# Kernel optimization log

Measured on AMD Instinct MI355X. Metric: run time of the kernel, lower is better.

Reference implementation:

```python
import jax, jax.numpy as jnp
import numpy as np

NEG = -1e9  # soft -inf, fp16/bf16-safe-ish and avoids nan from inf-inf


def _nw_single(theta, A):
    """Soft Needleman-Wunsch (softmax operator = logsumexp merge).

    theta: [N, M] match scores, A: scalar gap score.
    V is conceptually an (N+1, M+1) grid with V[0,0]=0 and -inf boundaries:
      V[i, j] = theta[i-1, j-1] + lse(V[i-1, j] + A, V[i-1, j-1], V[i, j-1] + A)
    Computed wavefront-parallel over anti-diagonals d = i + j with lax.scan.
    Each diagonal is a length-(N+1) vector indexed by row i.
    Returns V[N, M].
    """
    N, M = theta.shape
    neg = jnp.asarray(NEG, theta.dtype)
    ii = jnp.arange(N)  # ii = i - 1 for active rows i = 1..N

    prev2 = jnp.full((N + 1,), neg, theta.dtype).at[0].set(0.0)  # diagonal d=0
    prev = jnp.full((N + 1,), neg, theta.dtype)                   # diagonal d=1

    def step(carry, d):
        p2, p1 = carry
        jj = d - ii - 2                       # column index j-1 on diagonal d
        valid = (jj >= 0) & (jj < M)
        th = theta[ii, jnp.clip(jj, 0, M - 1)]
        up = p1[:N] + A                        # V[i-1, j] + A
        diag = p2[:N]                          # V[i-1, j-1]
        left = p1[1:] + A                      # V[i, j-1] + A
        merged = jax.nn.logsumexp(jnp.stack([up, diag, left]), axis=0)
        newvals = jnp.where(valid, th + merged, neg)
        new = jnp.concatenate([neg[None], newvals])  # row i=0 is boundary
        return (p1, new), None

    ds = jnp.arange(2, N + M + 1)
    (_, last), _ = jax.lax.scan(step, (prev2, prev), ds)
    return last[N]  # V[N, M], terminal alignment score


def setup_inputs() -> dict:
    key = jax.random.key(0)
    k1, k2, k3 = jax.random.split(key, 3)
    B, N, M, D = 16, 1024, 1024, 512
    zx = jax.random.normal(k1, (B, N, D), dtype=jnp.float32)
    zy = jax.random.normal(k2, (B, M, D), dtype=jnp.float32)
    gap_w = jax.random.normal(k3, (1, 2 * D), dtype=jnp.float32) * (1.0 / np.sqrt(2 * D))
    gap_b = jnp.zeros((1,), dtype=jnp.float32)
    return {"zx": zx, "zy": zy, "gap_w": gap_w, "gap_b": gap_b}


def reference(zx, zy, gap_w, gap_b):
    # Pairwise match scores theta[b,i,j] = <zx[b,i], zy[b,j]>
    theta = jnp.einsum('bid,bjd->bij', zx, zy)
    # Per-pair scalar gap score from mean-pooled embeddings
    merged = jnp.concatenate([zx.mean(axis=1), zy.mean(axis=1)], axis=1)  # [B, 2D]
    A = (merged @ gap_w.T + gap_b)[:, 0]                                   # [B]
    # Soft NW alignment score per batch element
    return jax.vmap(_nw_single)(theta, A)                                  # [B]
```

## Files before the change

### kernel.cpp

```cpp
#include <hip/hip_runtime.h>
#include <hip/hip_bf16.h>

#define BATCH 16
#define NN 1024
#define MM 1024
#define DD 512

#define LOG2E 1.4426950408889634f
#define LN2f  0.6931471805599453f
#define NEGS  -1.442695e9f

#define DSTAG 128
#define GTOT  1480
#define PF    8

typedef __bf16 v8bf __attribute__((ext_vector_type(8)));
typedef __bf16 v4bf __attribute__((ext_vector_type(4)));
typedef float  v4f  __attribute__((ext_vector_type(4)));

__global__ void zero_acc(float* a) {
    if (threadIdx.x < BATCH) a[threadIdx.x] = 0.0f;
}

__global__ __launch_bounds__(256) void conv_reduce(
        const float* __restrict__ zx, const float* __restrict__ zy,
        const float* __restrict__ gw,
        __bf16* __restrict__ zxb, __bf16* __restrict__ zyb,
        float* __restrict__ acc) {
    const int chunk = blockIdx.x, b = blockIdx.y, which = blockIdx.z;
    const float* src = which ? zy : zx;
    __bf16* dst = which ? zyb : zxb;
    const float* g = gw + which * DD;
    const size_t base = ((size_t)b * NN + (size_t)chunk * 64) * DD;
    const int t = threadIdx.x;
    const int col = (t * 4) & (DD - 1);
    const float4 gv = *(const float4*)(g + col);
    float sum = 0.0f;
    #pragma unroll 4
    for (int it = 0; it < 32; ++it) {
        size_t off = base + (size_t)it * 1024 + t * 4;
        float4 x = *(const float4*)(src + off);
        sum += x.x * gv.x + x.y * gv.y + x.z * gv.z + x.w * gv.w;
        v4bf o = { (__bf16)x.x, (__bf16)x.y, (__bf16)x.z, (__bf16)x.w };
        *(v4bf*)(dst + off) = o;
    }
    #pragma unroll
    for (int o = 32; o > 0; o >>= 1) sum += __shfl_down(sum, o);
    __shared__ float wsum[4];
    if ((t & 63) == 0) wsum[t >> 6] = sum;
    __syncthreads();
    if (t == 0) {
        float s = wsum[0] + wsum[1] + wsum[2] + wsum[3];
        atomicAdd(acc + b, s * (1.0f / 1024.0f));
    }
}

__global__ __launch_bounds__(256) void gemm_bt(
        const __bf16* __restrict__ Abf, const __bf16* __restrict__ Bbf,
        float* __restrict__ theta) {
    __shared__ __bf16 As[64 * 40];
    __shared__ __bf16 Bs[64 * 40];
    const int b = blockIdx.z;
    const int i0 = blockIdx.y * 64, j0 = blockIdx.x * 64;
    const __bf16* ap = Abf + ((size_t)b * NN + i0) * DD;
    const __bf16* bp = Bbf + ((size_t)b * MM + j0) * DD;
    const int t = threadIdx.x;
    const int srow = t >> 2, scol = (t & 3) * 8;
    const int lane = t & 63, wave = t >> 6;
    const int mrow = lane & 15, quad = lane >> 4;
    v4f acc[4] = {};
    for (int kk = 0; kk < DD; kk += 32) {
        if (kk) __syncthreads();
        *(v8bf*)&As[srow * 40 + scol] = *(const v8bf*)(ap + (size_t)srow * DD + kk + scol);
        *(v8bf*)&Bs[srow * 40 + scol] = *(const v8bf*)(bp + (size_t)srow * DD + kk + scol);
        __syncthreads();
        v8bf af = *(const v8bf*)&As[(wave * 16 + mrow) * 40 + quad * 8];
        #pragma unroll
        for (int tt = 0; tt < 4; ++tt) {
            v8bf bf = *(const v8bf*)&Bs[(tt * 16 + mrow) * 40 + quad * 8];
            acc[tt] = __builtin_amdgcn_mfma_f32_16x16x32_bf16(af, bf, acc[tt], 0, 0, 0);
        }
    }
    const size_t tb = (size_t)b * NN * MM;
    #pragma unroll
    for (int tt = 0; tt < 4; ++tt) {
        int j = j0 + tt * 16 + mrow;
        #pragma unroll
        for (int r = 0; r < 4; ++r) {
            int i = i0 + wave * 16 + quad * 4 + r;
            theta[tb + (size_t)i * MM + j] = acc[tt][r];
        }
    }
}

__global__ __launch_bounds__(256) void nw_dp(
        const float* __restrict__ thetaT, const float* __restrict__ acc,
        const float* __restrict__ gap_b, float* __restrict__ out) {
    const int b = blockIdx.x;
    const int tid = threadIdx.x;
    const int t = tid & 63, w = tid >> 6;
    const float Ac = (acc[b] + gap_b[0]) * LOG2E;
    const int row0 = w * 256 + t * 4;
    const int off = w * DSTAG + t;
    const float* Tb = thetaT + (size_t)b * NN * MM + row0;

    __shared__ float ring[3][256];

    float v[4];
    v[0] = v[1] = v[2] = v[3] = NEGS;
    float v3c = NEGS, v3p = NEGS;

    float4 pf[PF];
    #pragma unroll
    for (int u = 0; u < PF; ++u) {
        int c0 = u - off;
        c0 = c0 < 0 ? 0 : (c0 > MM - 1 ? MM - 1 : c0);
        pf[u] = *(const float4*)(Tb + (size_t)c0 * NN);
    }
    float rtc = NEGS, rtp = NEGS;

    for (int gg = 0; gg < GTOT; gg += PF) {
        #pragma unroll
        for (int u = 0; u < PF; ++u) {
            const int g = gg + u;
            const int c = g - off;
            float tc = __shfl_up(v3c, 1);
            float tp = __shfl_up(v3p, 1);
            if (t == 0) {
                if (w == 0) { tc = NEGS; tp = (c == 0) ? 0.0f : NEGS; }
                else        { tc = rtc;  tp = (c == 0) ? NEGS : rtp; }
            }
            v3p = v3c;

            const float4 cur = pf[u];
            int cn = g + PF - off;
            cn = cn < 0 ? 0 : (cn > MM - 1 ? MM - 1 : cn);
            pf[u] = *(const float4*)(Tb + (size_t)cn * NN);

            if (c >= 0 && c < MM) {
                const float* th = (const float*)&cur;
                float up_in = tc, dg = tp;
                #pragma unroll
                for (int k = 0; k < 4; ++k) {
                    float left = v[k];
                    float up = up_in + Ac;
                    float lf = left + Ac;
                    float mx = fmaxf(fmaxf(up, dg), lf);
                    float ss = __builtin_amdgcn_exp2f(up - mx)
                             + __builtin_amdgcn_exp2f(dg - mx)
                             + __builtin_amdgcn_exp2f(lf - mx);
                    float nv = fmaf(th[k], LOG2E, mx + __builtin_amdgcn_logf(ss));
                    dg = left;
                    up_in = nv;
                    v[k] = nv;
                }
                v3c = v[3];
                if (t == 63 && w < 3) ring[w][c & 255] = v[3];
            }

            if ((g & 63) == 63) __syncthreads();

            if (t == 0 && w > 0) {
                int cnx = g + 1 - off;
                rtc = ring[w - 1][cnx & 255];
                rtp = ring[w - 1][(cnx - 1) & 255];
            }
        }
    }
    if (tid == 255) out[b] = v[3] * LN2f;
}

extern "C" void kernel_launch(void* const* d_in, const int* in_sizes, int n_in,
                              void* d_out, int out_size, void* d_ws, size_t ws_size,
                              hipStream_t stream) {
    const float* zx    = (const float*)d_in[0];
    const float* zy    = (const float*)d_in[1];
    const float* gw    = (const float*)d_in[2];
    const float* gapb  = (const float*)d_in[3];
    float* out = (float*)d_out;

    char* ws = (char*)d_ws;
    float*  thetaT = (float*)ws;
    __bf16* zxb   = (__bf16*)(ws + (size_t)67108864);
    __bf16* zyb   = (__bf16*)(ws + (size_t)67108864 + 16777216);
    float*  acc   = (float*)(ws + (size_t)67108864 + 2 * 16777216);

    zero_acc<<<1, 64, 0, stream>>>(acc);
    conv_reduce<<<dim3(16, BATCH, 2), 256, 0, stream>>>(zx, zy, gw, zxb, zyb, acc);
    gemm_bt<<<dim3(MM / 64, NN / 64, BATCH), 256, 0, stream>>>(zyb, zxb, thetaT);
    nw_dp<<<BATCH, 256, 0, stream>>>(thetaT, acc, gapb, out);
}
```

Before: 519.4 us.

## Split NW wavefront over 8 waves with 2 rows per lane and DPP shifts

The DP kernel now uses 8 waves per batch element, each lane owning 2 rows instead of 4. This shortens the per-step serial chain at the cost of a longer wavefront (1760 steps), with waves staggered by 96 steps and a barrier every 32 steps. The lane shift uses a DPP row-shift instead of a ds_bpermute shuffle. The logsumexp is refactored to pull the gap term out as a multiplier, saving adds per cell. The inter-wave ring read is simplified to reuse the previous value. Risks include more barriers, extra fill and drain steps, and DPP row_shr semantics across 16-lane rows.

```diff
diff --git a/kernel.cpp b/kernel.cpp
--- a/kernel.cpp
+++ b/kernel.cpp
@@ -10,13 +10,21 @@
 #define LN2f  0.6931471805599453f
 #define NEGS  -1.442695e9f
 
-#define DSTAG 128
-#define GTOT  1480
+#define NWAVE 8
+#define DSTAG 96
+#define BARP  32
+#define GTOT  1760
 #define PF    8
 
 typedef __bf16 v8bf __attribute__((ext_vector_type(8)));
 typedef __bf16 v4bf __attribute__((ext_vector_type(4)));
 typedef float  v4f  __attribute__((ext_vector_type(4)));
+
+__device__ __forceinline__ float wave_shr1(float x) {
+    int xi = __float_as_int(x);
+    int r = __builtin_amdgcn_update_dpp(xi, xi, 0x138, 0xf, 0xf, false);
+    return __int_as_float(r);
+}
 
 __global__ void zero_acc(float* a) {
     if (threadIdx.x < BATCH) a[threadIdx.x] = 0.0f;
@@ -93,29 +101,29 @@
     }
 }
 
-__global__ __launch_bounds__(256) void nw_dp(
+__global__ __launch_bounds__(512) void nw_dp(
         const float* __restrict__ thetaT, const float* __restrict__ acc,
         const float* __restrict__ gap_b, float* __restrict__ out) {
     const int b = blockIdx.x;
     const int tid = threadIdx.x;
     const int t = tid & 63, w = tid >> 6;
     const float Ac = (acc[b] + gap_b[0]) * LOG2E;
-    const int row0 = w * 256 + t * 4;
+    const float Ka = __builtin_amdgcn_exp2f(Ac);
+    const int row0 = w * 128 + t * 2;
     const int off = w * DSTAG + t;
     const float* Tb = thetaT + (size_t)b * NN * MM + row0;
 
-    __shared__ float ring[3][256];
+    __shared__ float ring[NWAVE - 1][256];
 
-    float v[4];
-    v[0] = v[1] = v[2] = v[3] = NEGS;
-    float v3c = NEGS, v3p = NEGS;
+    float v0 = NEGS, v1 = NEGS;
+    float vbc = NEGS, vbp = NEGS;
 
-    float4 pf[PF];
+    float2 pf[PF];
     #pragma unroll
     for (int u = 0; u < PF; ++u) {
         int c0 = u - off;
         c0 = c0 < 0 ? 0 : (c0 > MM - 1 ? MM - 1 : c0);
-        pf[u] = *(const float4*)(Tb + (size_t)c0 * NN);
+        pf[u] = *(const float2*)(Tb + (size_t)c0 * NN);
     }
     float rtc = NEGS, rtp = NEGS;
 
@@ -124,50 +132,46 @@
         for (int u = 0; u < PF; ++u) {
             const int g = gg + u;
             const int c = g - off;
-            float tc = __shfl_up(v3c, 1);
-            float tp = __shfl_up(v3p, 1);
+            float tc = wave_shr1(vbc);
+            float tp = wave_shr1(vbp);
             if (t == 0) {
                 if (w == 0) { tc = NEGS; tp = (c == 0) ? 0.0f : NEGS; }
                 else        { tc = rtc;  tp = (c == 0) ? NEGS : rtp; }
             }
-            v3p = v3c;
+            vbp = vbc;
 
-            const float4 cur = pf[u];
+            const float2 cur = pf[u];
             int cn = g + PF - off;
             cn = cn < 0 ? 0 : (cn > MM - 1 ? MM - 1 : cn);
-            pf[u] = *(const float4*)(Tb + (size_t)cn * NN);
+            pf[u] = *(const float2*)(Tb + (size_t)cn * NN);
 
             if (c >= 0 && c < MM) {
-                const float* th = (const float*)&cur;
-                float up_in = tc, dg = tp;
-                #pragma unroll
-                for (int k = 0; k < 4; ++k) {
-                    float left = v[k];
-                    float up = up_in + Ac;
-                    float lf = left + Ac;
-                    float mx = fmaxf(fmaxf(up, dg), lf);
-                    float ss = __builtin_amdgcn_exp2f(up - mx)
-                             + __builtin_amdgcn_exp2f(dg - mx)
-                             + __builtin_amdgcn_exp2f(lf - mx);
-                    float nv = fmaf(th[k], LOG2E, mx + __builtin_amdgcn_logf(ss));
-                    dg = left;
-                    up_in = nv;
-                    v[k] = nv;
-                }
-                v3c = v[3];
-                if (t == 63 && w < 3) ring[w][c & 255] = v[3];
+                float mx0 = fmaxf(fmaxf(tc, v0), tp);
+                float e0a = __builtin_amdgcn_exp2f(tc - mx0);
+                float e0b = __builtin_amdgcn_exp2f(v0 - mx0);
+                float e0c = __builtin_amdgcn_exp2f(tp - mx0);
+                float s0  = fmaf(Ka, e0a + e0b, e0c);
+                float nv0 = fmaf(cur.x, LOG2E, mx0 + Ac + __builtin_amdgcn_logf(s0));
+                float mx1 = fmaxf(fmaxf(nv0, v1), v0);
+                float e1a = __builtin_amdgcn_exp2f(nv0 - mx1);
+                float e1b = __builtin_amdgcn_exp2f(v1 - mx1);
+                float e1c = __builtin_amdgcn_exp2f(v0 - mx1);
+                float s1  = fmaf(Ka, e1a + e1b, e1c);
+                float nv1 = fmaf(cur.y, LOG2E, mx1 + Ac + __builtin_amdgcn_logf(s1));
+                v0 = nv0; v1 = nv1;
+                vbc = nv1;
+                if (t == 63 && w < NWAVE - 1) ring[w][c & 255] = nv1;
             }
 
-            if ((g & 63) == 63) __syncthreads();
+            if ((g & (BARP - 1)) == (BARP - 1)) __syncthreads();
 
             if (t == 0 && w > 0) {
-                int cnx = g + 1 - off;
-                rtc = ring[w - 1][cnx & 255];
-                rtp = ring[w - 1][(cnx - 1) & 255];
+                rtp = rtc;
+                rtc = ring[w - 1][(g + 1 - off) & 255];
             }
         }
     }
-    if (tid == 255) out[b] = v[3] * LN2f;
+    if (tid == NWAVE * 64 - 1) out[b] = v1 * LN2f;
 }
 
 extern "C" void kernel_launch(void* const* d_in, const int* in_sizes, int n_in,
@@ -188,5 +192,5 @@
     zero_acc<<<1, 64, 0, stream>>>(acc);
     conv_reduce<<<dim3(16, BATCH, 2), 256, 0, stream>>>(zx, zy, gw, zxb, zyb, acc);
     gemm_bt<<<dim3(MM / 64, NN / 64, BATCH), 256, 0, stream>>>(zyb, zxb, thetaT);
-    nw_dp<<<BATCH, 256, 0, stream>>>(thetaT, acc, gapb, out);
+    nw_dp<<<BATCH, NWAVE * 64, 0, stream>>>(thetaT, acc, gapb, out);
 }
```

After: 660.9 us. 1.27x slower.

## Use DPP lane shift, pipelined ring reads, and pack two batches per NW block

Applied to the files above, without the earlier changes.

The wavefront DP kernel now uses a DPP row-shift instead of __shfl_up to pass boundary values between lanes. Each wave prefetches its upstream neighbor's ring values PF steps ahead into a register array, which takes the LDS read off the per-step critical path. To allow that lookahead, the inter-wave stagger grows (DSTAG 128 to 144) and so does the total step count. Two batch elements now share one 512-thread block, halving the number of blocks. The costs are extra steps from the wider stagger, and barriers that now couple two independent batches. The DPP control 0x138 is a wave_shr1, which on some architectures may not shift across 16-lane rows as expected, and wrong lane transfer would break correctness.

```diff
diff --git a/kernel.cpp b/kernel.cpp
--- a/kernel.cpp
+++ b/kernel.cpp
@@ -10,13 +10,20 @@
 #define LN2f  0.6931471805599453f
 #define NEGS  -1.442695e9f
 
-#define DSTAG 128
-#define GTOT  1480
+#define DSTAG 144
+#define BARP  64
+#define GTOT  1520
 #define PF    8
 
 typedef __bf16 v8bf __attribute__((ext_vector_type(8)));
 typedef __bf16 v4bf __attribute__((ext_vector_type(4)));
 typedef float  v4f  __attribute__((ext_vector_type(4)));
+
+__device__ __forceinline__ float wave_shr1(float x) {
+    int xi = __float_as_int(x);
+    int r = __builtin_amdgcn_update_dpp(xi, xi, 0x138, 0xf, 0xf, false);
+    return __int_as_float(r);
+}
 
 __global__ void zero_acc(float* a) {
     if (threadIdx.x < BATCH) a[threadIdx.x] = 0.0f;
@@ -93,22 +100,23 @@
     }
 }
 
-__global__ __launch_bounds__(256) void nw_dp(
+__global__ __launch_bounds__(512) void nw_dp(
         const float* __restrict__ thetaT, const float* __restrict__ acc,
         const float* __restrict__ gap_b, float* __restrict__ out) {
-    const int b = blockIdx.x;
     const int tid = threadIdx.x;
     const int t = tid & 63, w = tid >> 6;
+    const int grp = w >> 2, wg = w & 3;
+    const int b = blockIdx.x * 2 + grp;
     const float Ac = (acc[b] + gap_b[0]) * LOG2E;
-    const int row0 = w * 256 + t * 4;
-    const int off = w * DSTAG + t;
+    const int row0 = wg * 256 + t * 4;
+    const int off = wg * DSTAG + t;
     const float* Tb = thetaT + (size_t)b * NN * MM + row0;
 
-    __shared__ float ring[3][256];
+    __shared__ float ring[2][3][256];
 
     float v[4];
     v[0] = v[1] = v[2] = v[3] = NEGS;
-    float v3c = NEGS, v3p = NEGS;
+    float vbc = NEGS, vbp = NEGS;
 
     float4 pf[PF];
     #pragma unroll
@@ -117,20 +125,23 @@
         c0 = c0 < 0 ? 0 : (c0 > MM - 1 ? MM - 1 : c0);
         pf[u] = *(const float4*)(Tb + (size_t)c0 * NN);
     }
-    float rtc = NEGS, rtp = NEGS;
+    float rt[PF];
+    #pragma unroll
+    for (int u = 0; u < PF; ++u) rt[u] = NEGS;
+    float rtprev = NEGS;
 
     for (int gg = 0; gg < GTOT; gg += PF) {
         #pragma unroll
         for (int u = 0; u < PF; ++u) {
             const int g = gg + u;
             const int c = g - off;
-            float tc = __shfl_up(v3c, 1);
-            float tp = __shfl_up(v3p, 1);
+            float tc = wave_shr1(vbc);
+            float tp = wave_shr1(vbp);
             if (t == 0) {
-                if (w == 0) { tc = NEGS; tp = (c == 0) ? 0.0f : NEGS; }
-                else        { tc = rtc;  tp = (c == 0) ? NEGS : rtp; }
+                if (wg == 0) { tc = NEGS; tp = (c == 0) ? 0.0f : NEGS; }
+                else         { tc = rt[u]; tp = (c == 0) ? NEGS : rtprev; rtprev = rt[u]; }
             }
-            v3p = v3c;
+            vbp = vbc;
 
             const float4 cur = pf[u];
             int cn = g + PF - off;
@@ -154,20 +165,20 @@
                     up_in = nv;
                     v[k] = nv;
                 }
-                v3c = v[3];
-                if (t == 63 && w < 3) ring[w][c & 255] = v[3];
+                vbc = v[3];
+                if (t == 63 && wg < 3) ring[grp][wg][c & 255] = v[3];
             }
 
-            if ((g & 63) == 63) __syncthreads();
-
-            if (t == 0 && w > 0) {
-                int cnx = g + 1 - off;
-                rtc = ring[w - 1][cnx & 255];
-                rtp = ring[w - 1][(cnx - 1) & 255];
+            if ((g & (BARP - 1)) == (BARP - 1)) __syncthreads();
+
+            if (t == 0 && wg > 0) {
+                int cp = g + PF - off;
+                cp = cp < 0 ? 0 : (cp > MM - 1 ? MM - 1 : cp);
+                rt[u] = ring[grp][wg - 1][cp & 255];
             }
         }
     }
-    if (tid == 255) out[b] = v[3] * LN2f;
+    if (t == 63 && wg == 3) out[b] = v[3] * LN2f;
 }
 
 extern "C" void kernel_launch(void* const* d_in, const int* in_sizes, int n_in,
@@ -188,5 +199,5 @@
     zero_acc<<<1, 64, 0, stream>>>(acc);
     conv_reduce<<<dim3(16, BATCH, 2), 256, 0, stream>>>(zx, zy, gw, zxb, zyb, acc);
     gemm_bt<<<dim3(MM / 64, NN / 64, BATCH), 256, 0, stream>>>(zyb, zxb, thetaT);
-    nw_dp<<<BATCH, 256, 0, stream>>>(thetaT, acc, gapb, out);
-}
+    nw_dp<<<BATCH / 2, 512, 0, stream>>>(thetaT, acc, gapb, out);
+}
```

Result: slower. 794.3 us (+52.9%).
